# Kernel optimization log

Measured on AMD Instinct MI355X. Metric: run time of the kernel, lower is better.

Reference implementation:

```python
import jax, jax.numpy as jnp
import numpy as np

B, C, H, W = 8, 256, 128, 128
S = C // 4          # squeezed channels (squeeze_factor=4)
HEADS = 8

def _conv(x, w, pad, groups=1):
    # NCHW conv, stride 1
    return jax.lax.conv_general_dilated(
        x, w, (1, 1), [(pad, pad), (pad, pad)],
        feature_group_count=groups,
        dimension_numbers=('NCHW', 'OIHW', 'NCHW'))

def _cln(x, w, b):
    # WithBias LayerNorm over channel dim (to_3d -> LN over c -> to_4d)
    mu = jnp.mean(x, axis=1, keepdims=True)
    var = jnp.mean((x - mu) ** 2, axis=1, keepdims=True)
    return (x - mu) * jax.lax.rsqrt(var + 1e-5) * w[None, :, None, None] + b[None, :, None, None]

def setup_inputs() -> dict:
    key = jax.random.key(0)
    ks = jax.random.split(key, 14)
    r = lambda i, shape, s=0.05: jax.random.normal(ks[i], shape, jnp.float32) * s
    return dict(
        x=r(0, (B, C, H, W), 1.0),
        y=r(1, (B, C, H, W), 1.0),
        w_cq=r(2, (S, C, 3, 3)),          # compress_q
        w_ckv=r(3, (S, C, 3, 3)),         # compress_kv
        ln_q_w=jnp.ones(S), ln_q_b=jnp.zeros(S),
        ln_kv_w=jnp.ones(S), ln_kv_b=jnp.zeros(S),
        w_kv=r(4, (2 * S, S, 1, 1)),      # kv 1x1
        w_kvdw=r(5, (2 * S, 1, 3, 3)),    # kv depthwise 3x3
        w_q=r(6, (S, S, 3, 3)),           # q 3x3
        temperature=jnp.ones((HEADS, 1, 1)),
        w_po=r(7, (S, S, 1, 1)),          # project_out 1x1
        w_expand=r(8, (C, S, 3, 3)),      # expand 3x3
        ln_out_w=jnp.ones(C), ln_out_b=jnp.zeros(C),
        w_ffn1=r(9, (C, 2 * C, 1, 1)),    # ffn conv1x1 (dim_q+dim_kv -> dim_out)
        w_ffn_dw=r(10, (C, 1, 3, 3)),     # ffn depthwise 3x3
        w_ffn2=r(11, (C, C, 1, 1)),       # ffn conv1x1
    )

def reference(x, y, w_cq, w_ckv, ln_q_w, ln_q_b, ln_kv_w, ln_kv_b,
              w_kv, w_kvdw, w_q, temperature, w_po, w_expand,
              ln_out_w, ln_out_b, w_ffn1, w_ffn_dw, w_ffn2):
    # channel compress + LayerNorm
    xq = _cln(_conv(x, w_cq, 1), ln_q_w, ln_q_b)      # [B,S,H,W]
    ykv = _cln(_conv(y, w_ckv, 1), ln_kv_w, ln_kv_b)  # [B,S,H,W]
    b, c, h, w = xq.shape
    # cross channel attention
    kv = _conv(_conv(ykv, w_kv, 0), w_kvdw, 1, groups=2 * c)
    k, v = jnp.split(kv, 2, axis=1)
    q = _conv(xq, w_q, 1)
    sh = lambda t: t.reshape(b, HEADS, c // HEADS, h * w)  # b head c (hw)
    q, k, v = sh(q), sh(k), sh(v)
    q = q / jnp.maximum(jnp.linalg.norm(q, axis=-1, keepdims=True), 1e-12)
    k = k / jnp.maximum(jnp.linalg.norm(k, axis=-1, keepdims=True), 1e-12)
    attn = jax.nn.softmax(
        jnp.einsum('bhcn,bhdn->bhcd', q, k) * temperature[None], axis=-1)
    o = jnp.einsum('bhcd,bhdn->bhcn', attn, v).reshape(b, c, h, w)
    o = _conv(o, w_po, 0)
    # expand back to full channels, norm, conv FFN
    vexp = _conv(o, w_expand, 1)                      # [B,C,H,W]
    vn = _cln(vexp, ln_out_w, ln_out_b)
    cat = jnp.concatenate([x, vn], axis=1)            # [B,2C,H,W]
    f = _conv(cat, w_ffn1, 0)
    f = jax.nn.gelu(_conv(f, w_ffn_dw, 1, groups=f.shape[1]), approximate=False)
    return _conv(f, w_ffn2, 0)
```

## Files before the change

### kernel.cpp

```cpp
#include <hip/hip_runtime.h>
#include <hip/hip_bf16.h>
#include <math.h>

#define B_ 8
#define C_ 256
#define S_ 64
#define H_ 128
#define W_ 128
#define HW_ (H_*W_)
#define P_ (B_*HW_)

typedef __attribute__((ext_vector_type(8))) short short8;
typedef __attribute__((ext_vector_type(4))) float f32x4;

__device__ __forceinline__ unsigned short f2b(float f){
    __hip_bfloat16 h = __float2bfloat16(f);
    return *reinterpret_cast<unsigned short*>(&h);
}
__device__ __forceinline__ void up8(uint4 u, float* f){
    unsigned v0=u.x,v1=u.y,v2=u.z,v3=u.w;
    f[0]=__uint_as_float(v0<<16); f[1]=__uint_as_float(v0&0xffff0000u);
    f[2]=__uint_as_float(v1<<16); f[3]=__uint_as_float(v1&0xffff0000u);
    f[4]=__uint_as_float(v2<<16); f[5]=__uint_as_float(v2&0xffff0000u);
    f[6]=__uint_as_float(v3<<16); f[7]=__uint_as_float(v3&0xffff0000u);
}
__device__ __forceinline__ uint4 pk8(const float* f){
    uint4 u;
    u.x = (unsigned)f2b(f[0]) | ((unsigned)f2b(f[1])<<16);
    u.y = (unsigned)f2b(f[2]) | ((unsigned)f2b(f[3])<<16);
    u.z = (unsigned)f2b(f[4]) | ((unsigned)f2b(f[5])<<16);
    u.w = (unsigned)f2b(f[6]) | ((unsigned)f2b(f[7])<<16);
    return u;
}
__device__ __forceinline__ void gl2lds(const unsigned short* g, unsigned short* l){
    __builtin_amdgcn_global_load_lds((const __attribute__((address_space(1))) void*)g,
                                     (__attribute__((address_space(3))) void*)l, 16, 0, 0);
}

__global__ __launch_bounds__(256) void pack_k(const float* __restrict__ inA,
                                              const float* __restrict__ inB,
                                              unsigned short* __restrict__ outA,
                                              unsigned short* __restrict__ outB)
{
    __shared__ unsigned short tl[64][72];
    const int t = threadIdx.x;
    const int p0 = blockIdx.x*64, c0 = blockIdx.y*64;
    const int sel = blockIdx.z >> 3, b = blockIdx.z & 7;
    const float* in = sel ? inB : inA;
    unsigned short* out = sel ? outB : outA;
    const float* ib = in + ((size_t)b*C_ + c0)*HW_ + p0;
    for (int i = t; i < 1024; i += 256){
        int ci = i >> 4, px = (i & 15)*4;
        float4 v = *(const float4*)(ib + (size_t)ci*HW_ + px);
        tl[px+0][ci]=f2b(v.x); tl[px+1][ci]=f2b(v.y); tl[px+2][ci]=f2b(v.z); tl[px+3][ci]=f2b(v.w);
    }
    __syncthreads();
    unsigned short* ob = out + ((size_t)b*HW_ + p0)*C_ + c0;
    for (int i = t; i < 512; i += 256){
        int px = i >> 3, c8 = (i & 7)*8;
        *(uint4*)(ob + (size_t)px*C_ + c8) = *(uint4*)&tl[px][c8];
    }
}

__device__ __forceinline__ void packw(const float* __restrict__ src, unsigned short* __restrict__ dst,
                                      int e, int CO, int CI, int KS2)
{
    int KB = CI/32;
    int tap = e / (CO*CI);
    int rem = e % (CO*CI);
    int coT = rem / (CI*16);
    int rem2 = rem % (CI*16);
    int kb = rem2 >> 9;
    int l  = (rem2 >> 3) & 63;
    int ee = rem2 & 7;
    int co = coT*16 + (l & 15);
    int ci = kb*32 + (l >> 4)*8 + ee;
    float v = (KS2==9) ? src[(size_t)(co*CI+ci)*9 + tap] : src[(size_t)co*CI + ci];
    dst[e] = f2b(v);
}

__global__ __launch_bounds__(256) void prep_k(const float* __restrict__ cq, const float* __restrict__ ckv,
                                              const float* __restrict__ q,  const float* __restrict__ kv,
                                              const float* __restrict__ f1, const float* __restrict__ f2,
                                              const float* __restrict__ dwk, const float* __restrict__ dwf,
                                              unsigned short* o_cq, unsigned short* o_ckv, unsigned short* o_q,
                                              unsigned short* o_kv, unsigned short* o_f1, unsigned short* o_f2,
                                              unsigned short* o_dwk, unsigned short* o_dwf)
{
    int i = blockIdx.x*256 + threadIdx.x;
    if      (i < 147456) packw(cq,  o_cq,  i,          64, 256, 9);
    else if (i < 294912) packw(ckv, o_ckv, i-147456,   64, 256, 9);
    else if (i < 331776) packw(q,   o_q,   i-294912,   64,  64, 9);
    else if (i < 339968) packw(kv,  o_kv,  i-331776,  128,  64, 1);
    else if (i < 471040) packw(f1,  o_f1,  i-339968,  256, 512, 1);
    else if (i < 536576) packw(f2,  o_f2,  i-471040,  256, 256, 1);
    else if (i < 537728) { int e=i-536576; o_dwk[e] = f2b(dwk[(e&127)*9 + (e>>7)]); }
    else if (i < 540032) { int e=i-537728; o_dwf[e] = f2b(dwf[(e&255)*9 + (e>>8)]); }
    else if (i < 540040) { o_dwf[i-537728] = 0; }
}

template<int C0,int C1,int COUT,int KS,int OUTM,int LNF>
__global__ __launch_bounds__(256,4) void mconv_k(
    const unsigned short* __restrict__ in0, int s0,
    const unsigned short* __restrict__ in1, int s1,
    const unsigned short* __restrict__ wp, long wpbs,
    void* __restrict__ outp, int so,
    const unsigned short* __restrict__ in0B,
    const unsigned short* __restrict__ wpB2,
    void* __restrict__ outB,
    const unsigned short* __restrict__ zbuf,
    const float* __restrict__ lnw0, const float* __restrict__ lnb0,
    const float* __restrict__ lnw1, const float* __restrict__ lnb1)
{
    constexpr int CINT = C0+C1;
    constexpr int KB  = CINT/32;
    constexpr int MT  = 4;
    constexpr int NT  = 2;
    constexpr int RWS = (KS==3)?4:1;
    constexpr int PXS = (KS==3)?66:128;
    constexpr int NTR = RWS*PXS*4;
    constexpr int NLD = (NTR+255)/256;
    constexpr int ASZ = RWS*PXS*32;
    constexpr int EP  = (OUTM==1) ? 64*132*2 : 128*64;
    constexpr int SSZ = (2*ASZ > EP) ? 2*ASZ : EP;
    __shared__ alignas(16) unsigned short sbuf[SSZ];

    const int t = threadIdx.x;
    const int sel = blockIdx.z >> 3;
    const int b   = blockIdx.z & 7;
    const int cob = blockIdx.y*64;
    const size_t pb = (size_t)b*HW_;
    const unsigned short* pin0 = sel ? in0B : in0;
    const unsigned short* wpb  = (sel ? wpB2 : wp) + (size_t)b*wpbs;

    int y0=0,x0=0; size_t p0=0;
    if (KS==3){ y0=(blockIdx.x>>1)*2; x0=(blockIdx.x&1)*64; }
    else p0 = (size_t)blockIdx.x*128;

    const int l = t&63, w = t>>6;
    const int wy = w>>1, wx = w&1;
    const int lrow = l&15, lk = l>>4;

    auto issueA = [&](int kb, int bsel){
        const int cg = kb*32;
        unsigned short* dst = sbuf + bsel*ASZ;
        #pragma unroll
        for (int j=0;j<NLD;++j){
            int i = t + j*256;
            if ((NTR%256)==0 || j<NLD-1 || i<NTR){
                int slot = i&3, pr = i>>2;
                int px = pr%PXS, row = pr/PXS;
                int g = slot ^ (px&3);
                int c = cg + g*8;
                const unsigned short* sp;
                if (KS==3){
                    int gy = y0+row-1, gx = x0+px-1;
                    bool ok = ((unsigned)gy<(unsigned)H_) & ((unsigned)gx<(unsigned)W_);
                    size_t p = (size_t)gy*W_+gx;
                    const unsigned short* base = (c<C0)? pin0+(pb+p)*s0+c : in1+(pb+p)*s1+(c-C0);
                    sp = ok ? base : zbuf;
                } else {
                    size_t p = p0+px;
                    sp = (c<C0)? pin0+(pb+p)*s0+c : in1+(pb+p)*s1+(c-C0);
                }
                gl2lds(sp, dst + (size_t)i*8);
            }
        }
    };
    auto loadB = [&](short8* dst, int kb, int tap){
        #pragma unroll
        for (int n=0;n<NT;++n){
            int fi = (tap*(COUT/16) + (cob>>4) + wx*NT + n)*KB + kb;
            dst[n] = *(const short8*)(wpb + (size_t)fi*512 + l*8);
        }
    };

    f32x4 acc[MT][NT] = {};

    if (KS==3){
        short8 bfs[3][NT];
        issueA(0,0);
        loadB(bfs[0],0,0); loadB(bfs[1],0,1); loadB(bfs[2],0,2);
        for (int kb=0; kb<KB; ++kb){
            __syncthreads();
            unsigned short* cur = sbuf + (kb&1)*ASZ;
            #pragma unroll
            for (int tap=0;tap<9;++tap){
                const int ky=tap/3, kx=tap%3;
                if (tap==2 && kb+1<KB) issueA(kb+1,(kb+1)&1);
                short8 af[MT];
                #pragma unroll
                for (int m=0;m<MT;++m){
                    int pl = wy*64 + m*16 + lrow;
                    int r = (pl>>6)+ky, xx = (pl&63)+kx;
                    af[m] = *(const short8*)&cur[((r*PXS+xx)*4 + (lk^(xx&3)))*8];
                }
                #pragma unroll
                for (int m=0;m<MT;++m)
                    #pragma unroll
                    for (int n=0;n<NT;++n)
                        acc[m][n] = __builtin_amdgcn_mfma_f32_16x16x32_bf16(af[m],bfs[tap%3][n],acc[m][n],0,0,0);
                if (tap+3 < 9)      loadB(bfs[tap%3], kb, tap+3);
                else if (kb+1<KB)   loadB(bfs[tap%3], kb+1, tap-6);
            }
        }
    } else {
        short8 bfs[2][NT];
        issueA(0,0);
        loadB(bfs[0],0,0); if (KB>1) loadB(bfs[1],1,0);
        auto step1 = [&](int kb, short8 (&bcur)[NT]){
            __syncthreads();
            unsigned short* cur = sbuf + (kb&1)*ASZ;
            if (kb+1<KB) issueA(kb+1,(kb+1)&1);
            short8 af[MT];
            #pragma unroll
            for (int m=0;m<MT;++m){
                int pl = wy*64 + m*16 + lrow;
                af[m] = *(const short8*)&cur[(pl*4 + (lk^(pl&3)))*8];
            }
            #pragma unroll
            for (int m=0;m<MT;++m)
                #pragma unroll
                for (int n=0;n<NT;++n)
                    acc[m][n] = __builtin_amdgcn_mfma_f32_16x16x32_bf16(af[m],bcur[n],acc[m][n],0,0,0);
            if (kb+2<KB) loadB(bcur, kb+2, 0);
        };
        for (int kb2=0; kb2<KB; kb2+=2){
            step1(kb2,   bfs[0]);
            step1(kb2+1, bfs[1]);
        }
    }
    __syncthreads();

    if (OUTM==1){
        float* sf = (float*)sbuf;
        #pragma unroll
        for (int m=0;m<MT;++m)
            #pragma unroll
            for (int n=0;n<NT;++n){
                int co_l = wx*32 + n*16 + lrow;
                int pl0  = wy*64 + m*16 + lk*4;
                *(f32x4*)&sf[co_l*132 + pl0] = acc[m][n];
            }
        __syncthreads();
        float* out = (float*)(sel ? outB : outp);
        for (int i=t; i<2048; i+=256){
            int co = i>>5, pxg = i&31;
            f32x4 v = *(const f32x4*)&sf[co*132 + pxg*4];
            *(f32x4*)(out + ((size_t)(b*COUT + cob + co))*HW_ + p0 + pxg*4) = v;
        }
    } else if (LNF){
        #pragma unroll
        for (int m=0;m<MT;++m)
            #pragma unroll
            for (int n=0;n<NT;++n){
                int co = wx*32 + n*16 + lrow;
                int grp = co>>3, cr = co&7;
                #pragma unroll
                for (int r=0;r<4;++r){
                    int pl = wy*64 + m*16 + lk*4 + r;
                    sbuf[pl*64 + ((grp^(pl&7))<<3) + cr] = f2b(acc[m][n][r]);
                }
            }
        __syncthreads();
        if (t < 128){
            int pl = t;
            uint4 raw[8];
            float s = 0.f, ss = 0.f;
            #pragma unroll
            for (int j=0;j<8;++j){
                raw[j] = *(const uint4*)&sbuf[pl*64 + ((j^(pl&7))<<3)];
                float f[8]; up8(raw[j], f);
                #pragma unroll
                for (int k=0;k<8;++k){ s += f[k]; ss += f[k]*f[k]; }
            }
            float mu = s*(1.f/64.f);
            float rs = rsqrtf(ss*(1.f/64.f) - mu*mu + 1e-5f);
            const float* lw = sel ? lnw1 : lnw0;
            const float* lb = sel ? lnb1 : lnb0;
            unsigned short* out = (unsigned short*)(sel ? outB : outp);
            size_t p = (size_t)(y0+(pl>>6))*W_ + x0 + (pl&63);
            unsigned short* orow = out + (pb+p)*64;
            #pragma unroll
            for (int j=0;j<8;++j){
                float f[8], o[8];
                up8(raw[j], f);
                #pragma unroll
                for (int k=0;k<8;++k) o[k] = (f[k]-mu)*rs*lw[j*8+k] + lb[j*8+k];
                *(uint4*)(orow + j*8) = pk8(o);
            }
        }
    } else {
        unsigned short* out = (unsigned short*)(sel ? outB : outp);
        #pragma unroll
        for (int m=0;m<MT;++m)
            #pragma unroll
            for (int n=0;n<NT;++n){
                int co = wx*32 + n*16 + lrow;
                #pragma unroll
                for (int r=0;r<4;++r){
                    int pl = wy*64 + m*16 + lk*4 + r;
                    sbuf[pl*64 + co] = f2b(acc[m][n][r]);
                }
            }
        __syncthreads();
        for (int i=t; i<1024; i+=256){
            int pl = i>>3, c8 = (i&7)*8;
            size_t p = (KS==3) ? ((size_t)(y0+(pl>>6))*W_ + (size_t)(x0+(pl&63))) : (p0+pl);
            *(uint4*)(out + (pb+p)*so + cob + c8) = *(uint4*)&sbuf[pl*64 + c8];
        }
    }
}

template<int C>
__global__ __launch_bounds__(256) void cln_k(unsigned short* __restrict__ io,
                                             const float* __restrict__ wg,
                                             const float* __restrict__ bi)
{
    constexpr int L = C/8;
    size_t idx = (size_t)blockIdx.x*256 + threadIdx.x;
    int sub = (int)(idx % L);
    size_t pix = idx / L;
    unsigned short* rp = io + pix*C + (size_t)sub*8;
    uint4 raw = *(const uint4*)rp;
    float f[8]; up8(raw, f);
    float s = 0.f, ss = 0.f;
    #pragma unroll
    for (int j=0;j<8;++j){ s += f[j]; ss += f[j]*f[j]; }
    #pragma unroll
    for (int m=1;m<L;m<<=1){ s += __shfl_xor(s,m); ss += __shfl_xor(ss,m); }
    float mu = s*(1.f/C);
    float rs = rsqrtf(ss*(1.f/C) - mu*mu + 1e-5f);
    float4 w0 = *(const float4*)(wg+sub*8), w1 = *(const float4*)(wg+sub*8+4);
    float4 b0 = *(const float4*)(bi+sub*8), b1 = *(const float4*)(bi+sub*8+4);
    float o[8];
    o[0]=(f[0]-mu)*rs*w0.x+b0.x; o[1]=(f[1]-mu)*rs*w0.y+b0.y;
    o[2]=(f[2]-mu)*rs*w0.z+b0.z; o[3]=(f[3]-mu)*rs*w0.w+b0.w;
    o[4]=(f[4]-mu)*rs*w1.x+b1.x; o[5]=(f[5]-mu)*rs*w1.y+b1.y;
    o[6]=(f[6]-mu)*rs*w1.z+b1.z; o[7]=(f[7]-mu)*rs*w1.w+b1.w;
    *(uint4*)rp = pk8(o);
}

template<int CH, bool GELU>
__global__ __launch_bounds__(256) void dw_k(const unsigned short* __restrict__ in,
                                            const unsigned short* __restrict__ wp,
                                            unsigned short* __restrict__ out)
{
    size_t idx = (size_t)blockIdx.x*256 + threadIdx.x;
    int c8 = (int)(idx % (CH/8));
    size_t pix = idx / (CH/8);
    int p = (int)(pix % HW_);
    size_t pb = pix - p;
    int yy = p >> 7, xx = p & 127;
    float wf[9][8];
    #pragma unroll
    for (int tap=0; tap<9; ++tap){
        uint4 r = *(const uint4*)(wp + tap*CH + c8*8);
        up8(r, wf[tap]);
    }
    float a[8] = {0,0,0,0,0,0,0,0};
    #pragma unroll
    for (int ky=0; ky<3; ++ky){
        int gy = yy+ky-1;
        if ((unsigned)gy >= (unsigned)H_) continue;
        #pragma unroll
        for (int kx=0; kx<3; ++kx){
            int gx = xx+kx-1;
            if ((unsigned)gx >= (unsigned)W_) continue;
            uint4 r = *(const uint4*)(in + (pb + (size_t)gy*W_ + gx)*CH + c8*8);
            float f[8]; up8(r, f);
            #pragma unroll
            for (int j=0;j<8;++j) a[j] += f[j]*wf[ky*3+kx][j];
        }
    }
    if (GELU){
        #pragma unroll
        for (int j=0;j<8;++j) a[j] = 0.5f*a[j]*(1.f + erff(a[j]*0.70710678118654752f));
    }
    *(uint4*)(out + pix*CH + c8*8) = pk8(a);
}

__global__ __launch_bounds__(256) void attn_k(const unsigned short* __restrict__ qc,
                                              const unsigned short* __restrict__ kvd,
                                              const float* __restrict__ temp,
                                              float* __restrict__ probs)
{
    int b = blockIdx.x >> 3, h = blockIdx.x & 7;
    int t = threadIdx.x;
    const unsigned short* qb = qc  + (size_t)b*HW_*64  + h*8;
    const unsigned short* kb = kvd + (size_t)b*HW_*128 + h*8;
    float qs[8] = {}, ks[8] = {}, dt[8][8] = {{}};
    for (int p = t; p < HW_; p += 256){
        float qv[8], kv[8];
        up8(*(const uint4*)(qb + (size_t)p*64),  qv);
        up8(*(const uint4*)(kb + (size_t)p*128), kv);
        #pragma unroll
        for (int i=0;i<8;++i){ qs[i]+=qv[i]*qv[i]; ks[i]+=kv[i]*kv[i]; }
        #pragma unroll
        for (int i=0;i<8;++i)
            #pragma unroll
            for (int j=0;j<8;++j) dt[i][j] += qv[i]*kv[j];
    }
    __shared__ float red[4][80];
    __shared__ float fin[80];
    int lane = t & 63, wv = t >> 6;
    #pragma unroll
    for (int i=0;i<8;++i){ float v=qs[i]; for (int m=1;m<64;m<<=1) v += __shfl_xor(v,m); if(!lane) red[wv][i]=v; }
    #pragma unroll
    for (int i=0;i<8;++i){ float v=ks[i]; for (int m=1;m<64;m<<=1) v += __shfl_xor(v,m); if(!lane) red[wv][8+i]=v; }
    #pragma unroll
    for (int i=0;i<8;++i)
        #pragma unroll
        for (int j=0;j<8;++j){ float v=dt[i][j]; for (int m=1;m<64;m<<=1) v += __shfl_xor(v,m); if(!lane) red[wv][16+i*8+j]=v; }
    __syncthreads();
    if (t < 80) fin[t] = red[0][t]+red[1][t]+red[2][t]+red[3][t];
    __syncthreads();
    if (t < 8){
        int i = t;
        float qn = fmaxf(sqrtf(fin[i]), 1e-12f);
        float tm = temp[h];
        float lg[8]; float mx = -1e30f;
        #pragma unroll
        for (int j=0;j<8;++j){
            float kn = fmaxf(sqrtf(fin[8+j]), 1e-12f);
            lg[j] = fin[16+i*8+j]/(qn*kn)*tm;
            mx = fmaxf(mx, lg[j]);
        }
        float se = 0.f;
        #pragma unroll
        for (int j=0;j<8;++j){ lg[j]=expf(lg[j]-mx); se+=lg[j]; }
        float inv = 1.f/se;
        #pragma unroll
        for (int j=0;j<8;++j) probs[(((size_t)b*8+h)*8+i)*8+j] = lg[j]*inv;
    }
}

__global__ __launch_bounds__(256) void mb_k(const float* __restrict__ probs,
                                            const float* __restrict__ wpo,
                                            float* __restrict__ Mb)
{
    int b = blockIdx.x;
    for (int o = threadIdx.x; o < 4096; o += 256){
        int co = o >> 6, d = o & 63, h = d >> 3, j = d & 7;
        float s = 0.f;
        #pragma unroll
        for (int i2=0;i2<8;++i2)
            s += wpo[co*64 + h*8 + i2] * probs[(((size_t)b*8+h)*8+i2)*8 + j];
        Mb[(size_t)b*4096 + o] = s;
    }
}

__global__ __launch_bounds__(256) void weff_k(const float* __restrict__ Mb,
                                              const float* __restrict__ wex,
                                              unsigned short* __restrict__ weff)
{
    int b = blockIdx.x / 576;
    int i = (blockIdx.x % 576)*256 + threadIdx.x;
    int tap = i / 16384;
    int rem = i % 16384;
    int coT = rem / 1024;
    int rem2 = rem % 1024;
    int kb = rem2 >> 9;
    int l  = (rem2 >> 3) & 63;
    int ee = rem2 & 7;
    int eo = coT*16 + (l & 15);
    int d  = kb*32 + (l >> 4)*8 + ee;
    const float* mb = Mb + (size_t)b*4096;
    float s = 0.f;
    #pragma unroll 8
    for (int c=0;c<64;++c)
        s += wex[(size_t)(eo*64+c)*9 + tap] * mb[c*64 + d];
    weff[(size_t)b*147456 + i] = f2b(s);
}

extern "C" void kernel_launch(void* const* d_in, const int* in_sizes, int n_in,
                              void* d_out, int out_size, void* d_ws, size_t ws_size,
                              hipStream_t stream) {
    (void)in_sizes; (void)n_in; (void)out_size; (void)ws_size;
    const float* x        = (const float*)d_in[0];
    const float* y        = (const float*)d_in[1];
    const float* w_cq     = (const float*)d_in[2];
    const float* w_ckv    = (const float*)d_in[3];
    const float* ln_q_w   = (const float*)d_in[4];
    const float* ln_q_b   = (const float*)d_in[5];
    const float* ln_kv_w  = (const float*)d_in[6];
    const float* ln_kv_b  = (const float*)d_in[7];
    const float* w_kv     = (const float*)d_in[8];
    const float* w_kvdw   = (const float*)d_in[9];
    const float* w_q      = (const float*)d_in[10];
    const float* temperature = (const float*)d_in[11];
    const float* w_po     = (const float*)d_in[12];
    const float* w_expand = (const float*)d_in[13];
    const float* ln_out_w = (const float*)d_in[14];
    const float* ln_out_b = (const float*)d_in[15];
    const float* w_ffn1   = (const float*)d_in[16];
    const float* w_ffn_dw = (const float*)d_in[17];
    const float* w_ffn2   = (const float*)d_in[18];
    float* outp = (float*)d_out;

    const size_t MB = 1u<<20;
    char* ws8 = (char*)d_ws;
    unsigned short* ykv  = (unsigned short*)(ws8 + 0);
    unsigned short* xq   = (unsigned short*)(ws8 + 16*MB);
    unsigned short* kv1  = (unsigned short*)(ws8 + 32*MB);
    unsigned short* qc   = (unsigned short*)(ws8 + 64*MB);
    unsigned short* kvd  = (unsigned short*)(ws8 + 80*MB);
    unsigned short* vexp = (unsigned short*)(ws8 + 0);
    unsigned short* f2b_ = (unsigned short*)(ws8 + 0);
    float* probs = (float*)(ws8 + 112*MB);
    float* Mb    = (float*)(ws8 + 113*MB);
    unsigned short* weff = (unsigned short*)(ws8 + 114*MB);
    unsigned short* wpB  = (unsigned short*)(ws8 + 117*MB);
    unsigned short* wp_cq  = wpB;
    unsigned short* wp_ckv = wpB + 147456;
    unsigned short* wp_q   = wpB + 294912;
    unsigned short* wp_kv  = wpB + 331776;
    unsigned short* wp_f1  = wpB + 339968;
    unsigned short* wp_f2  = wpB + 471040;
    unsigned short* wp_dwk = wpB + 536576;
    unsigned short* wp_dwf = wpB + 537728;
    unsigned short* zbuf   = wpB + 540032;
    unsigned short* xb = (unsigned short*)d_out;
    unsigned short* yb = (unsigned short*)d_out + 32*MB;
    unsigned short* f1 = yb;

    const unsigned short* NUL = (const unsigned short*)nullptr;

    prep_k<<<2111, 256, 0, stream>>>(w_cq, w_ckv, w_q, w_kv, w_ffn1, w_ffn2, w_kvdw, w_ffn_dw,
                                     wp_cq, wp_ckv, wp_q, wp_kv, wp_f1, wp_f2, wp_dwk, wp_dwf);
    pack_k<<<dim3(256,4,16), 256, 0, stream>>>(y, x, yb, xb);
    mconv_k<256,0,64,3,0,1><<<dim3(128,1,16), 256, 0, stream>>>(yb,256, NUL,0, wp_ckv,0, ykv,64,
        xb, wp_cq, xq, zbuf, ln_kv_w, ln_kv_b, ln_q_w, ln_q_b);
    mconv_k<64,0,128,1,0,0><<<dim3(128,2,8), 256, 0, stream>>>(ykv,64, NUL,0, wp_kv,0, kv1,128,
        ykv, wp_kv, kv1, zbuf, NULL,NULL,NULL,NULL);
    mconv_k<64,0,64,3,0,0><<<dim3(128,1,8), 256, 0, stream>>>(xq,64, NUL,0, wp_q,0, qc,64,
        xq, wp_q, qc, zbuf, NULL,NULL,NULL,NULL);
    dw_k<128,false><<<8192, 256, 0, stream>>>(kv1, wp_dwk, kvd);
    attn_k<<<64, 256, 0, stream>>>(qc, kvd, temperature, probs);
    mb_k<<<8, 256, 0, stream>>>(probs, w_po, Mb);
    weff_k<<<4608, 256, 0, stream>>>(Mb, w_expand, weff);
    mconv_k<64,0,256,3,0,0><<<dim3(128,4,8), 256, 0, stream>>>(kvd+64,128, NUL,0, weff,147456, vexp,256,
        kvd+64, weff, vexp, zbuf, NULL,NULL,NULL,NULL);
    cln_k<256><<<16384, 256, 0, stream>>>(vexp, ln_out_w, ln_out_b);
    mconv_k<256,256,256,1,0,0><<<dim3(128,4,8), 256, 0, stream>>>(xb,256, vexp,256, wp_f1,0, f1,256,
        xb, wp_f1, f1, zbuf, NULL,NULL,NULL,NULL);
    dw_k<256,true><<<16384, 256, 0, stream>>>(f1, wp_dwf, f2b_);
    mconv_k<256,0,256,1,1,0><<<dim3(128,4,8), 256, 0, stream>>>(f2b_,256, NUL,0, wp_f2,0, outp,0,
        f2b_, wp_f2, outp, zbuf, NULL,NULL,NULL,NULL);
}
```

Before: 617.0 us.

## Switch activations to channel-blocked NHWC32 layout and swizzle block order across XCDs

Activations are now stored in blocks of 32 channels, each block laid out contiguously over pixels ([b][c/32][hw][32]) instead of full NHWC. Every kernel (pack, mconv, cln, dw, attn) is rewritten to use the new indexing. The aim is to shorten load strides and make the per-k-block A loads more contiguous. Separately, the mconv grid is flattened to 1D and block ids are remapped so that consecutive blocks go to different XCDs (blockIdx&7), for better L2 locality. This touches every kernel, which raises the risk of indexing mistakes, and the 1x1 conv A loads now stride across channel blocks.

```diff
diff --git a/kernel.cpp b/kernel.cpp
--- a/kernel.cpp
+++ b/kernel.cpp
@@ -36,6 +36,7 @@
     __builtin_amdgcn_global_load_lds((const __attribute__((address_space(1))) void*)g,
                                      (__attribute__((address_space(3))) void*)l, 16, 0, 0);
 }
+
 
 __global__ __launch_bounds__(256) void pack_k(const float* __restrict__ inA,
                                               const float* __restrict__ inB,
@@ -55,10 +56,12 @@
         tl[px+0][ci]=f2b(v.x); tl[px+1][ci]=f2b(v.y); tl[px+2][ci]=f2b(v.z); tl[px+3][ci]=f2b(v.w);
     }
     __syncthreads();
-    unsigned short* ob = out + ((size_t)b*HW_ + p0)*C_ + c0;
     for (int i = t; i < 512; i += 256){
         int px = i >> 3, c8 = (i & 7)*8;
-        *(uint4*)(ob + (size_t)px*C_ + c8) = *(uint4*)&tl[px][c8];
+        int cc = c0 + c8;
+        unsigned short* dst = out + ((size_t)b*8 + (cc>>5))*(size_t)HW_*32
+                                  + (size_t)(p0+px)*32 + (cc&31);
+        *(uint4*)dst = *(uint4*)&tl[px][c8];
     }
 }
 
@@ -110,7 +113,8 @@
     void* __restrict__ outB,
     const unsigned short* __restrict__ zbuf,
     const float* __restrict__ lnw0, const float* __restrict__ lnb0,
-    const float* __restrict__ lnw1, const float* __restrict__ lnb1)
+    const float* __restrict__ lnw1, const float* __restrict__ lnb1,
+    int ny, int nz)
 {
     constexpr int CINT = C0+C1;
     constexpr int KB  = CINT/32;
@@ -126,20 +130,29 @@
     __shared__ alignas(16) unsigned short sbuf[SSZ];
 
     const int t = threadIdx.x;
-    const int sel = blockIdx.z >> 3;
-    const int b   = blockIdx.z & 7;
-    const int cob = blockIdx.y*64;
-    const size_t pb = (size_t)b*HW_;
+    const int nper = (128*ny*nz) >> 3;
+    int lin = (blockIdx.x & 7)*nper + (blockIdx.x >> 3);
+    const int gy_ = lin % ny;
+    int rem = lin / ny;
+    const int gx_ = rem & 127;
+    const int gz_ = rem >> 7;
+    const int sel = gz_ >> 3;
+    const int b   = gz_ & 7;
+    const int cob = gy_*64;
+
     const unsigned short* pin0 = sel ? in0B : in0;
     const unsigned short* wpb  = (sel ? wpB2 : wp) + (size_t)b*wpbs;
 
     int y0=0,x0=0; size_t p0=0;
-    if (KS==3){ y0=(blockIdx.x>>1)*2; x0=(blockIdx.x&1)*64; }
-    else p0 = (size_t)blockIdx.x*128;
+    if (KS==3){ y0=(gx_>>1)*2; x0=(gx_&1)*64; }
+    else p0 = (size_t)gx_*128;
 
     const int l = t&63, w = t>>6;
     const int wy = w>>1, wx = w&1;
     const int lrow = l&15, lk = l>>4;
+
+    const size_t b0base = (size_t)b*HW_*s0;
+    const size_t b1base = (size_t)b*HW_*s1;
 
     auto issueA = [&](int kb, int bsel){
         const int cg = kb*32;
@@ -157,11 +170,15 @@
                     int gy = y0+row-1, gx = x0+px-1;
                     bool ok = ((unsigned)gy<(unsigned)H_) & ((unsigned)gx<(unsigned)W_);
                     size_t p = (size_t)gy*W_+gx;
-                    const unsigned short* base = (c<C0)? pin0+(pb+p)*s0+c : in1+(pb+p)*s1+(c-C0);
+                    const unsigned short* base = (c<C0)
+                        ? pin0 + b0base + ((size_t)(c>>5)*HW_ + p)*32 + (c&31)
+                        : in1  + b1base + ((size_t)((c-C0)>>5)*HW_ + p)*32 + ((c-C0)&31);
                     sp = ok ? base : zbuf;
                 } else {
                     size_t p = p0+px;
-                    sp = (c<C0)? pin0+(pb+p)*s0+c : in1+(pb+p)*s1+(c-C0);
+                    sp = (c<C0)
+                        ? pin0 + b0base + ((size_t)(c>>5)*HW_ + p)*32 + (c&31)
+                        : in1  + b1base + ((size_t)((c-C0)>>5)*HW_ + p)*32 + ((c-C0)&31);
                 }
                 gl2lds(sp, dst + (size_t)i*8);
             }
@@ -280,14 +297,15 @@
             const float* lb = sel ? lnb1 : lnb0;
             unsigned short* out = (unsigned short*)(sel ? outB : outp);
             size_t p = (size_t)(y0+(pl>>6))*W_ + x0 + (pl&63);
-            unsigned short* orow = out + (pb+p)*64;
             #pragma unroll
             for (int j=0;j<8;++j){
                 float f[8], o[8];
                 up8(raw[j], f);
                 #pragma unroll
                 for (int k=0;k<8;++k) o[k] = (f[k]-mu)*rs*lw[j*8+k] + lb[j*8+k];
-                *(uint4*)(orow + j*8) = pk8(o);
+                int cc = j*8;
+                unsigned short* dst = out + ((size_t)b*2 + (cc>>5))*(size_t)HW_*32 + p*32 + (cc&31);
+                *(uint4*)dst = pk8(o);
             }
         }
     } else {
@@ -307,7 +325,9 @@
         for (int i=t; i<1024; i+=256){
             int pl = i>>3, c8 = (i&7)*8;
             size_t p = (KS==3) ? ((size_t)(y0+(pl>>6))*W_ + (size_t)(x0+(pl&63))) : (p0+pl);
-            *(uint4*)(out + (pb+p)*so + cob + c8) = *(uint4*)&sbuf[pl*64 + c8];
+            int cc = cob + c8;
+            unsigned short* dst = out + (size_t)b*HW_*so + ((size_t)(cc>>5)*HW_ + p)*32 + (cc&31);
+            *(uint4*)dst = *(uint4*)&sbuf[pl*64 + c8];
         }
     }
 }
@@ -321,7 +341,9 @@
     size_t idx = (size_t)blockIdx.x*256 + threadIdx.x;
     int sub = (int)(idx % L);
     size_t pix = idx / L;
-    unsigned short* rp = io + pix*C + (size_t)sub*8;
+    int b = (int)(pix >> 14);
+    size_t p = pix & (HW_-1);
+    unsigned short* rp = io + ((size_t)b*(C/32) + (sub>>2))*(size_t)HW_*32 + p*32 + (sub&3)*8;
     uint4 raw = *(const uint4*)rp;
     float f[8]; up8(raw, f);
     float s = 0.f, ss = 0.f;
@@ -350,8 +372,9 @@
     int c8 = (int)(idx % (CH/8));
     size_t pix = idx / (CH/8);
     int p = (int)(pix % HW_);
-    size_t pb = pix - p;
+    int b = (int)(pix / HW_);
     int yy = p >> 7, xx = p & 127;
+    const unsigned short* ib = in + ((size_t)b*(CH/32) + (c8>>2))*(size_t)HW_*32 + (c8&3)*8;
     float wf[9][8];
     #pragma unroll
     for (int tap=0; tap<9; ++tap){
@@ -367,7 +390,7 @@
         for (int kx=0; kx<3; ++kx){
             int gx = xx+kx-1;
             if ((unsigned)gx >= (unsigned)W_) continue;
-            uint4 r = *(const uint4*)(in + (pb + (size_t)gy*W_ + gx)*CH + c8*8);
+            uint4 r = *(const uint4*)(ib + (size_t)(gy*W_+gx)*32);
             float f[8]; up8(r, f);
             #pragma unroll
             for (int j=0;j<8;++j) a[j] += f[j]*wf[ky*3+kx][j];
@@ -377,7 +400,8 @@
         #pragma unroll
         for (int j=0;j<8;++j) a[j] = 0.5f*a[j]*(1.f + erff(a[j]*0.70710678118654752f));
     }
-    *(uint4*)(out + pix*CH + c8*8) = pk8(a);
+    unsigned short* ob = out + ((size_t)b*(CH/32) + (c8>>2))*(size_t)HW_*32 + (size_t)p*32 + (c8&3)*8;
+    *(uint4*)ob = pk8(a);
 }
 
 __global__ __launch_bounds__(256) void attn_k(const unsigned short* __restrict__ qc,
@@ -387,13 +411,13 @@
 {
     int b = blockIdx.x >> 3, h = blockIdx.x & 7;
     int t = threadIdx.x;
-    const unsigned short* qb = qc  + (size_t)b*HW_*64  + h*8;
-    const unsigned short* kb = kvd + (size_t)b*HW_*128 + h*8;
+    const unsigned short* qb = qc  + ((size_t)b*2 + (h>>2))*(size_t)HW_*32 + (h&3)*8;
+    const unsigned short* kb = kvd + ((size_t)b*4 + (h>>2))*(size_t)HW_*32 + (h&3)*8;
     float qs[8] = {}, ks[8] = {}, dt[8][8] = {{}};
     for (int p = t; p < HW_; p += 256){
         float qv[8], kv[8];
-        up8(*(const uint4*)(qb + (size_t)p*64),  qv);
-        up8(*(const uint4*)(kb + (size_t)p*128), kv);
+        up8(*(const uint4*)(qb + (size_t)p*32), qv);
+        up8(*(const uint4*)(kb + (size_t)p*32), kv);
         #pragma unroll
         for (int i=0;i<8;++i){ qs[i]+=qv[i]*qv[i]; ks[i]+=kv[i]*kv[i]; }
         #pragma unroll
@@ -529,22 +553,22 @@
     prep_k<<<2111, 256, 0, stream>>>(w_cq, w_ckv, w_q, w_kv, w_ffn1, w_ffn2, w_kvdw, w_ffn_dw,
                                      wp_cq, wp_ckv, wp_q, wp_kv, wp_f1, wp_f2, wp_dwk, wp_dwf);
     pack_k<<<dim3(256,4,16), 256, 0, stream>>>(y, x, yb, xb);
-    mconv_k<256,0,64,3,0,1><<<dim3(128,1,16), 256, 0, stream>>>(yb,256, NUL,0, wp_ckv,0, ykv,64,
-        xb, wp_cq, xq, zbuf, ln_kv_w, ln_kv_b, ln_q_w, ln_q_b);
-    mconv_k<64,0,128,1,0,0><<<dim3(128,2,8), 256, 0, stream>>>(ykv,64, NUL,0, wp_kv,0, kv1,128,
-        ykv, wp_kv, kv1, zbuf, NULL,NULL,NULL,NULL);
-    mconv_k<64,0,64,3,0,0><<<dim3(128,1,8), 256, 0, stream>>>(xq,64, NUL,0, wp_q,0, qc,64,
-        xq, wp_q, qc, zbuf, NULL,NULL,NULL,NULL);
+    mconv_k<256,0,64,3,0,1><<<128*1*16, 256, 0, stream>>>(yb,256, NUL,0, wp_ckv,0, ykv,64,
+        xb, wp_cq, xq, zbuf, ln_kv_w, ln_kv_b, ln_q_w, ln_q_b, 1, 16);
+    mconv_k<64,0,128,1,0,0><<<128*2*8, 256, 0, stream>>>(ykv,64, NUL,0, wp_kv,0, kv1,128,
+        ykv, wp_kv, kv1, zbuf, NULL,NULL,NULL,NULL, 2, 8);
+    mconv_k<64,0,64,3,0,0><<<128*1*8, 256, 0, stream>>>(xq,64, NUL,0, wp_q,0, qc,64,
+        xq, wp_q, qc, zbuf, NULL,NULL,NULL,NULL, 1, 8);
     dw_k<128,false><<<8192, 256, 0, stream>>>(kv1, wp_dwk, kvd);
     attn_k<<<64, 256, 0, stream>>>(qc, kvd, temperature, probs);
     mb_k<<<8, 256, 0, stream>>>(probs, w_po, Mb);
     weff_k<<<4608, 256, 0, stream>>>(Mb, w_expand, weff);
-    mconv_k<64,0,256,3,0,0><<<dim3(128,4,8), 256, 0, stream>>>(kvd+64,128, NUL,0, weff,147456, vexp,256,
-        kvd+64, weff, vexp, zbuf, NULL,NULL,NULL,NULL);
+    mconv_k<64,0,256,3,0,0><<<128*4*8, 256, 0, stream>>>(kvd + (size_t)HW_*64,128, NUL,0, weff,147456, vexp,256,
+        kvd + (size_t)HW_*64, weff, vexp, zbuf, NULL,NULL,NULL,NULL, 4, 8);
     cln_k<256><<<16384, 256, 0, stream>>>(vexp, ln_out_w, ln_out_b);
-    mconv_k<256,256,256,1,0,0><<<dim3(128,4,8), 256, 0, stream>>>(xb,256, vexp,256, wp_f1,0, f1,256,
-        xb, wp_f1, f1, zbuf, NULL,NULL,NULL,NULL);
+    mconv_k<256,256,256,1,0,0><<<128*4*8, 256, 0, stream>>>(xb,256, vexp,256, wp_f1,0, f1,256,
+        xb, wp_f1, f1, zbuf, NULL,NULL,NULL,NULL, 4, 8);
     dw_k<256,true><<<16384, 256, 0, stream>>>(f1, wp_dwf, f2b_);
-    mconv_k<256,0,256,1,1,0><<<dim3(128,4,8), 256, 0, stream>>>(f2b_,256, NUL,0, wp_f2,0, outp,0,
-        f2b_, wp_f2, outp, zbuf, NULL,NULL,NULL,NULL);
-}
+    mconv_k<256,0,256,1,1,0><<<128*4*8, 256, 0, stream>>>(f2b_,256, NUL,0, wp_f2,0, outp,0,
+        f2b_, wp_f2, outp, zbuf, NULL,NULL,NULL,NULL, 4, 8);
+}
```

Result: faster. 578.1 us (-6.3%).
